# Optimization experiments

Hardware: AMD Instinct MI355X
Metric: run time of the kernel (lower is better)

The kernel has to match this reference:

```python
import jax, jax.numpy as jnp
import numpy as np

N_NODES = 1_000_000
D_IN = 64
D_HID = 64
NUM_RATINGS = 10


def setup_inputs() -> dict:
    key = jax.random.key(0)
    k1, k2, k3, k4 = jax.random.split(key, 4)
    embed = jax.random.normal(k1, (N_NODES, D_IN), dtype=jnp.float32)
    # rating-indexed weight matrices W_r : (hidden_size, input_size)
    weights = jax.random.normal(k2, (NUM_RATINGS, D_HID, D_IN), dtype=jnp.float32)
    # precomputed 1/c_ij per edge (sqrt of neighbor-count product inverse)
    inv_c = jax.random.uniform(k3, (N_NODES,), dtype=jnp.float32)
    edge_node = jnp.arange(N_NODES, dtype=jnp.int64)
    edge_rating = jax.random.randint(k4, (N_NODES,), 0, NUM_RATINGS, dtype=jnp.int64)
    return {"embed": embed, "weights": weights, "inv_c": inv_c,
            "edge_node": edge_node, "edge_rating": edge_rating}


def reference(embed, weights, inv_c, edge_node, edge_rating):
    # gather per-edge source embeddings: [E, D_in]
    x = embed[edge_node]
    num_ratings, d_hid, _ = weights.shape
    # rating-specific matvec without materializing per-edge [Dh, Din] weights:
    # loop over the small fixed rating set, select per edge.
    h = jnp.zeros((x.shape[0], d_hid), dtype=x.dtype)
    for r in range(num_ratings):
        yr = x @ weights[r].T  # [E, Dh]
        h = jnp.where((edge_rating == r)[:, None], yr, h)
    h = h * inv_c[:, None]
    out = jnp.zeros((embed.shape[0], d_hid), dtype=x.dtype).at[edge_node].set(h)
    return out
```

## Files before the change

kernel.cpp:

```cpp
#include <hip/hip_runtime.h>
#include <hip/hip_bf16.h>

#define NUM_RATINGS 10

typedef short bf16x8 __attribute__((ext_vector_type(8)));
typedef float f32x4 __attribute__((ext_vector_type(4)));

static __device__ __forceinline__ bf16x8 rne8(float4 a, float4 b) {
    float f[8] = {a.x, a.y, a.z, a.w, b.x, b.y, b.z, b.w};
    union { unsigned short us[8]; bf16x8 v; } U;
    #pragma unroll
    for (int i = 0; i < 8; ++i) {
        unsigned u = __float_as_uint(f[i]);
        U.us[i] = (unsigned short)((u + 0x7fffu + ((u >> 16) & 1u)) >> 16);
    }
    return U.v;
}

__global__ void k_wfrag(const float* __restrict__ w, bf16x8* __restrict__ wf) {
    int r = blockIdx.x;
    int lane = threadIdx.x & 63;
    int eh = lane & 15, kg = lane >> 4;
    #pragma unroll
    for (int j = 0; j < 8; ++j) {
        int tt = j >> 1, ks = j & 1;
        const float4* p = reinterpret_cast<const float4*>(
            w + ((size_t)r << 12) + (size_t)(16 * tt + eh) * 64 + 32 * ks + 8 * kg);
        wf[(r * 8 + j) * 64 + lane] = rne8(p[0], p[1]);
    }
}

__global__ __launch_bounds__(256) void k_main(
    const float* __restrict__ embed, const bf16x8* __restrict__ wf,
    const float* __restrict__ invc, const int* __restrict__ enode,
    const int* __restrict__ erating, float* __restrict__ out, int E) {

    int lane = threadIdx.x & 63;
    int wv = threadIdx.x >> 6;
    int eh = lane & 15, kg = lane >> 4;
    int e0 = (blockIdx.x * 4 + wv) * 64;
    if (e0 >= E) return;

    int nd[4]; int rt[4]; float sc[4];
    #pragma unroll
    for (int it = 0; it < 4; ++it) {
        int et = e0 + 16 * it + eh;
        if (et > E - 1) et = E - 1;
        nd[it] = enode[et];
        rt[it] = erating[et];
        sc[it] = invc[et];
    }

    bf16x8 a0[4], a1[4];
    #pragma unroll
    for (int it = 0; it < 4; ++it) {
        const float4* xp = reinterpret_cast<const float4*>(embed + ((size_t)nd[it] << 6));
        float4 x0 = xp[2 * kg],     x1 = xp[2 * kg + 1];
        float4 x2 = xp[8 + 2 * kg], x3 = xp[9 + 2 * kg];
        a0[it] = rne8(x0, x1);
        a1[it] = rne8(x2, x3);
    }

    f32x4 acc[4][4];
    #pragma unroll
    for (int it = 0; it < 4; ++it)
        #pragma unroll
        for (int tt = 0; tt < 4; ++tt) acc[it][tt] = (f32x4){0.f, 0.f, 0.f, 0.f};

    #pragma unroll 1
    for (int r = 0; r < NUM_RATINGS; ++r) {
        bf16x8 B[8];
        #pragma unroll
        for (int j = 0; j < 8; ++j) B[j] = wf[(r * 8 + j) * 64 + lane];
        #pragma unroll
        for (int it = 0; it < 4; ++it) {
            bool m = (rt[it] == r);
            bf16x8 z = (bf16x8)(short)0;
            bf16x8 am0 = m ? a0[it] : z;
            bf16x8 am1 = m ? a1[it] : z;
            #pragma unroll
            for (int tt = 0; tt < 4; ++tt) {
                acc[it][tt] = __builtin_amdgcn_mfma_f32_16x16x32_bf16(am0, B[2 * tt],     acc[it][tt], 0, 0, 0);
                acc[it][tt] = __builtin_amdgcn_mfma_f32_16x16x32_bf16(am1, B[2 * tt + 1], acc[it][tt], 0, 0, 0);
            }
        }
    }

    int kg4 = kg << 2;
    #pragma unroll
    for (int it = 0; it < 4; ++it) {
        #pragma unroll
        for (int rg = 0; rg < 4; ++rg) {
            int er = e0 + 16 * it + kg4 + rg;
            int nd2 = __shfl(nd[it], kg4 + rg, 64);
            float s2 = __shfl(sc[it], kg4 + rg, 64);
            if (er < E) {
                float* po = out + ((size_t)nd2 << 6) + eh;
                __builtin_nontemporal_store(acc[it][0][rg] * s2, po);
                __builtin_nontemporal_store(acc[it][1][rg] * s2, po + 16);
                __builtin_nontemporal_store(acc[it][2][rg] * s2, po + 32);
                __builtin_nontemporal_store(acc[it][3][rg] * s2, po + 48);
            }
        }
    }
}

extern "C" void kernel_launch(void* const* d_in, const int* in_sizes, int n_in,
                              void* d_out, int out_size, void* d_ws, size_t ws_size,
                              hipStream_t stream) {
    const float* embed   = (const float*)d_in[0];
    const float* weights = (const float*)d_in[1];
    const float* invc    = (const float*)d_in[2];
    const int*   enode   = (const int*)d_in[3];
    const int*   erating = (const int*)d_in[4];
    float* out = (float*)d_out;

    int E = in_sizes[3];

    bf16x8* wf = (bf16x8*)d_ws;

    hipLaunchKernelGGL(k_wfrag, dim3(NUM_RATINGS), dim3(64), 0, stream, weights, wf);

    int waves = (E + 63) / 64;
    int blocks = (waves + 3) / 4;
    hipLaunchKernelGGL(k_main, dim3(blocks), dim3(256), 0, stream,
                       embed, wf, invc, enode, erating, out, E);
}
```

Baseline: 129.3 us.

## Bucket edges by rating in shared memory to avoid masked MFMAs across ratings

Each block now takes a 1024-edge window, builds a per-rating histogram with shared atomics, and places edge metadata (node, inv_c) into 16-aligned rating buckets in LDS. Each wave then walks its share of 16-edge tiles, reloading weight fragments only when the rating changes and issuing MFMAs for that one rating, instead of running all ten ratings with masked inputs. The inv_c scale is folded into the bf16 conversion of the input, and the next tile's embedding is prefetched. The cost is extra shared-memory setup, several block barriers, padding tiles per rating, and less parallelism per block, since each wave handles about 18 tiles in sequence. Folding the scale in before rounding slightly changes the numerics.

```diff
diff --git a/kernel.cpp b/kernel.cpp
--- a/kernel.cpp
+++ b/kernel.cpp
@@ -2,6 +2,8 @@
 #include <hip/hip_bf16.h>
 
 #define NUM_RATINGS 10
+#define WIN 1024
+#define MAXT 74
 
 typedef short bf16x8 __attribute__((ext_vector_type(8)));
 typedef float f32x4 __attribute__((ext_vector_type(4)));
@@ -12,6 +14,17 @@
     #pragma unroll
     for (int i = 0; i < 8; ++i) {
         unsigned u = __float_as_uint(f[i]);
+        U.us[i] = (unsigned short)((u + 0x7fffu + ((u >> 16) & 1u)) >> 16);
+    }
+    return U.v;
+}
+
+static __device__ __forceinline__ bf16x8 rne8s(float4 a, float4 b, float s) {
+    float f[8] = {a.x, a.y, a.z, a.w, b.x, b.y, b.z, b.w};
+    union { unsigned short us[8]; bf16x8 v; } U;
+    #pragma unroll
+    for (int i = 0; i < 8; ++i) {
+        unsigned u = __float_as_uint(f[i] * s);
         U.us[i] = (unsigned short)((u + 0x7fffu + ((u >> 16) & 1u)) >> 16);
     }
     return U.v;
@@ -35,73 +48,117 @@
     const float* __restrict__ invc, const int* __restrict__ enode,
     const int* __restrict__ erating, float* __restrict__ out, int E) {
 
-    int lane = threadIdx.x & 63;
-    int wv = threadIdx.x >> 6;
+    __shared__ int2 smeta[MAXT * 16];
+    __shared__ int shist[NUM_RATINGS];
+    __shared__ int spoff[NUM_RATINGS + 1];
+
+    int tid = threadIdx.x;
+    int base = blockIdx.x * WIN;
+
+    if (tid < NUM_RATINGS) shist[tid] = 0;
+    for (int i = tid; i < MAXT * 16; i += 256) smeta[i] = make_int2(-1, 0);
+    __syncthreads();
+
+    int er[4], rr[4], kk[4];
+    #pragma unroll
+    for (int i = 0; i < 4; ++i) {
+        int e = base + i * 256 + tid;
+        er[i] = e;
+        if (e < E) {
+            rr[i] = erating[e];
+            kk[i] = atomicAdd(&shist[rr[i]], 1);
+        }
+    }
+    __syncthreads();
+    if (tid == 0) {
+        int s = 0;
+        #pragma unroll
+        for (int r = 0; r < NUM_RATINGS; ++r) { spoff[r] = s; s += (shist[r] + 15) & ~15; }
+        spoff[NUM_RATINGS] = s;
+    }
+    __syncthreads();
+    #pragma unroll
+    for (int i = 0; i < 4; ++i)
+        if (er[i] < E)
+            smeta[spoff[rr[i]] + kk[i]] =
+                make_int2(enode[er[i]], __float_as_int(invc[er[i]]));
+    __syncthreads();
+
+    int pf1 = spoff[1], pf2 = spoff[2], pf3 = spoff[3], pf4 = spoff[4];
+    int pf5 = spoff[5], pf6 = spoff[6], pf7 = spoff[7], pf8 = spoff[8];
+    int pf9 = spoff[9];
+    int Tp = spoff[NUM_RATINGS] >> 4;
+
+    int lane = tid & 63, wv = tid >> 6;
     int eh = lane & 15, kg = lane >> 4;
-    int e0 = (blockIdx.x * 4 + wv) * 64;
-    if (e0 >= E) return;
 
-    int nd[4]; int rt[4]; float sc[4];
-    #pragma unroll
-    for (int it = 0; it < 4; ++it) {
-        int et = e0 + 16 * it + eh;
-        if (et > E - 1) et = E - 1;
-        nd[it] = enode[et];
-        rt[it] = erating[et];
-        sc[it] = invc[et];
+    int tpw = (Tp + 3) >> 2;
+    int t0 = wv * tpw;
+    int t1 = t0 + tpw; if (t1 > Tp) t1 = Tp;
+    if (t0 >= t1) return;
+
+    int2 mc = smeta[(t0 << 4) + eh];
+    {
+        int ndc = mc.x < 0 ? 0 : mc.x;
+        const float4* xp = reinterpret_cast<const float4*>(embed + ((size_t)ndc << 6));
+        (void)xp;
     }
+    const float4* xp0 = reinterpret_cast<const float4*>(
+        embed + ((size_t)(mc.x < 0 ? 0 : mc.x) << 6));
+    float4 xc0 = xp0[2 * kg], xc1 = xp0[2 * kg + 1];
+    float4 xc2 = xp0[8 + 2 * kg], xc3 = xp0[9 + 2 * kg];
 
-    bf16x8 a0[4], a1[4];
-    #pragma unroll
-    for (int it = 0; it < 4; ++it) {
-        const float4* xp = reinterpret_cast<const float4*>(embed + ((size_t)nd[it] << 6));
-        float4 x0 = xp[2 * kg],     x1 = xp[2 * kg + 1];
-        float4 x2 = xp[8 + 2 * kg], x3 = xp[9 + 2 * kg];
-        a0[it] = rne8(x0, x1);
-        a1[it] = rne8(x2, x3);
-    }
+    int cur_r = -1;
+    bf16x8 B[8];
 
-    f32x4 acc[4][4];
-    #pragma unroll
-    for (int it = 0; it < 4; ++it)
+    for (int t = t0; t < t1; ++t) {
+        int tn = (t + 1 < t1) ? t + 1 : t;
+        int2 mn = smeta[(tn << 4) + eh];
+        const float4* xq = reinterpret_cast<const float4*>(
+            embed + ((size_t)(mn.x < 0 ? 0 : mn.x) << 6));
+        float4 xn0 = xq[2 * kg], xn1 = xq[2 * kg + 1];
+        float4 xn2 = xq[8 + 2 * kg], xn3 = xq[9 + 2 * kg];
+
+        int tslot = t << 4;
+        int r = 0;
+        r += tslot >= pf1; r += tslot >= pf2; r += tslot >= pf3;
+        r += tslot >= pf4; r += tslot >= pf5; r += tslot >= pf6;
+        r += tslot >= pf7; r += tslot >= pf8; r += tslot >= pf9;
+        if (r != cur_r) {
+            cur_r = r;
+            #pragma unroll
+            for (int j = 0; j < 8; ++j) B[j] = wf[(r * 8 + j) * 64 + lane];
+        }
+
+        float s_ = mc.x < 0 ? 0.f : __int_as_float(mc.y);
+        bf16x8 a0 = rne8s(xc0, xc1, s_);
+        bf16x8 a1 = rne8s(xc2, xc3, s_);
+
+        f32x4 acc[4];
         #pragma unroll
-        for (int tt = 0; tt < 4; ++tt) acc[it][tt] = (f32x4){0.f, 0.f, 0.f, 0.f};
+        for (int tt = 0; tt < 4; ++tt) acc[tt] = (f32x4){0.f, 0.f, 0.f, 0.f};
+        #pragma unroll
+        for (int tt = 0; tt < 4; ++tt) {
+            acc[tt] = __builtin_amdgcn_mfma_f32_16x16x32_bf16(a0, B[2 * tt],     acc[tt], 0, 0, 0);
+            acc[tt] = __builtin_amdgcn_mfma_f32_16x16x32_bf16(a1, B[2 * tt + 1], acc[tt], 0, 0, 0);
+        }
 
-    #pragma unroll 1
-    for (int r = 0; r < NUM_RATINGS; ++r) {
-        bf16x8 B[8];
+        int vnd = mc.x;
+        int kg4 = kg << 2;
         #pragma unroll
-        for (int j = 0; j < 8; ++j) B[j] = wf[(r * 8 + j) * 64 + lane];
-        #pragma unroll
-        for (int it = 0; it < 4; ++it) {
-            bool m = (rt[it] == r);
-            bf16x8 z = (bf16x8)(short)0;
-            bf16x8 am0 = m ? a0[it] : z;
-            bf16x8 am1 = m ? a1[it] : z;
-            #pragma unroll
-            for (int tt = 0; tt < 4; ++tt) {
-                acc[it][tt] = __builtin_amdgcn_mfma_f32_16x16x32_bf16(am0, B[2 * tt],     acc[it][tt], 0, 0, 0);
-                acc[it][tt] = __builtin_amdgcn_mfma_f32_16x16x32_bf16(am1, B[2 * tt + 1], acc[it][tt], 0, 0, 0);
+        for (int rg = 0; rg < 4; ++rg) {
+            int nd2 = __shfl(vnd, kg4 + rg, 64);
+            if (nd2 >= 0) {
+                float* po = out + ((size_t)nd2 << 6) + eh;
+                __builtin_nontemporal_store(acc[0][rg], po);
+                __builtin_nontemporal_store(acc[1][rg], po + 16);
+                __builtin_nontemporal_store(acc[2][rg], po + 32);
+                __builtin_nontemporal_store(acc[3][rg], po + 48);
             }
         }
-    }
 
-    int kg4 = kg << 2;
-    #pragma unroll
-    for (int it = 0; it < 4; ++it) {
-        #pragma unroll
-        for (int rg = 0; rg < 4; ++rg) {
-            int er = e0 + 16 * it + kg4 + rg;
-            int nd2 = __shfl(nd[it], kg4 + rg, 64);
-            float s2 = __shfl(sc[it], kg4 + rg, 64);
-            if (er < E) {
-                float* po = out + ((size_t)nd2 << 6) + eh;
-                __builtin_nontemporal_store(acc[it][0][rg] * s2, po);
-                __builtin_nontemporal_store(acc[it][1][rg] * s2, po + 16);
-                __builtin_nontemporal_store(acc[it][2][rg] * s2, po + 32);
-                __builtin_nontemporal_store(acc[it][3][rg] * s2, po + 48);
-            }
-        }
+        mc = mn;
+        xc0 = xn0; xc1 = xn1; xc2 = xn2; xc3 = xn3;
     }
 }
 
@@ -121,8 +178,7 @@
 
     hipLaunchKernelGGL(k_wfrag, dim3(NUM_RATINGS), dim3(64), 0, stream, weights, wf);
 
-    int waves = (E + 63) / 64;
-    int blocks = (waves + 3) / 4;
-    hipLaunchKernelGGL(k_main, dim3(blocks), dim3(256), 0, stream,
+    int nW = (E + WIN - 1) / WIN;
+    hipLaunchKernelGGL(k_main, dim3(nW), dim3(256), 0, stream,
                        embed, wf, invc, enode, erating, out, E);
 }
```

Result: faster. 124.7 us (-3.6%).
